# Optimization experiments

Hardware: AMD Instinct MI355X
Metric: run time of the kernel (lower is better)

## Reference

```python
import jax, jax.numpy as jnp
import numpy as np

# Config (matches init_kwargs defaults): V=25 joints, C=16 -> D=400, heads=2,
# ffn=64*25=1600, window L=9, stride=1, postnorm, gelu, dropout ignored (eval).
N, C, T, V = 16, 16, 300, 25
D = C * V          # 400
H = 2              # nhead
FF = 64 * V        # 1600
L = 9              # trans_length
MAX_LEN = 301


def _layernorm(x, g, b, eps=1e-5):
    mu = jnp.mean(x, axis=-1, keepdims=True)
    var = jnp.mean(jnp.square(x - mu), axis=-1, keepdims=True)
    return (x - mu) * jax.lax.rsqrt(var + eps) * g + b


def setup_inputs() -> dict:
    key = jax.random.key(0)
    ks = jax.random.split(key, 12)
    s = 0.02
    return {
        "x": jax.random.normal(ks[0], (N, C, T, V), jnp.float32),
        "pe": jax.random.normal(ks[1], (1, MAX_LEN, D), jnp.float32) * s,
        "w_in": jax.random.normal(ks[2], (3 * D, D), jnp.float32) * s,
        "b_in": jnp.zeros((3 * D,), jnp.float32),
        "w_out": jax.random.normal(ks[3], (D, D), jnp.float32) * s,
        "b_out": jnp.zeros((D,), jnp.float32),
        "w1": jax.random.normal(ks[4], (FF, D), jnp.float32) * s,
        "b1": jnp.zeros((FF,), jnp.float32),
        "w2": jax.random.normal(ks[5], (D, FF), jnp.float32) * s,
        "b2": jnp.zeros((D,), jnp.float32),
        "ln1_g": jnp.ones((D,), jnp.float32),
        "ln1_b": jnp.zeros((D,), jnp.float32),
        "ln2_g": jnp.ones((D,), jnp.float32),
        "ln2_b": jnp.zeros((D,), jnp.float32),
    }


def _encoder_layer(h, w_in, b_in, w_out, b_out, w1, b1, w2, b2,
                   ln1_g, ln1_b, ln2_g, ln2_b):
    # h: [B, L, D]; post-norm TransformerEncoderLayer (torch default)
    B, Lw, Dm = h.shape
    dh = Dm // H
    qkv = h @ w_in.T + b_in                             # [B,L,3D]
    q, k, v = jnp.split(qkv, 3, axis=-1)
    def heads(t):
        return t.reshape(B, Lw, H, dh).transpose(0, 2, 1, 3)  # [B,H,L,dh]
    q, k, v = heads(q), heads(k), heads(v)
    scores = jnp.einsum('bhqd,bhkd->bhqk', q, k) / np.float32(np.sqrt(dh))
    att = jax.nn.softmax(scores, axis=-1)
    o = jnp.einsum('bhqk,bhkd->bhqd', att, v)
    o = o.transpose(0, 2, 1, 3).reshape(B, Lw, Dm) @ w_out.T + b_out
    h = _layernorm(h + o, ln1_g, ln1_b)
    ff = jax.nn.gelu(h @ w1.T + b1, approximate=False) @ w2.T + b2
    return _layernorm(h + ff, ln2_g, ln2_b)


def reference(x, pe, w_in, b_in, w_out, b_out, w1, b1, w2, b2,
              ln1_g, ln1_b, ln2_g, ln2_b):
    n, c, t, v = x.shape
    d = c * v
    # [N,C,T,V] -> [N,T,V,C] -> [N,T,D]  (flatten order is (V,C), as in torch view)
    xs = x.transpose(0, 2, 3, 1).reshape(n, t, d)
    xs = xs + pe[:, :t, :]
    W = t - L                                            # number of windows (stride=1)
    win = jnp.arange(W)
    idx = win[:, None] + jnp.arange(L)[None, :]          # [W,L] gather indices
    xw = xs[:, idx, :].reshape(n * W, L, d)              # batched windows
    out = _encoder_layer(xw, w_in, b_in, w_out, b_out, w1, b1, w2, b2,
                         ln1_g, ln1_b, ln2_g, ln2_b)
    out = out.reshape(n, W * L, d)
    # window i writes into rows i//2 : i//2 + L and results are summed
    pos = ((win // 2)[:, None] + jnp.arange(L)[None, :]).reshape(-1)  # [W*L]
    xt = jnp.zeros((n, t, d), xs.dtype).at[:, pos, :].add(out)
    # [N,T,D] -> [N,T,V,C] -> [N,C,T,V]
    return xt.reshape(n, t, v, c).transpose(0, 3, 1, 2)
```

## Files before the change

### kernel.cpp

```cpp
#include <hip/hip_runtime.h>
#include <cstdint>
#include <cstddef>

#define N_    16
#define C_    16
#define T_    300
#define V_    25
#define D_    400
#define H_    2
#define DH_   200
#define FF_   1600
#define L_    9
#define W_    291
#define NW_   (N_*W_)
#define NT_   (N_*T_)

#define KP_   416
#define SD_   400
#define SQKV_ 1200
#define SFF_  1600

#define WIN_OFF   0u
#define WOUT_OFF  1064960u
#define W1_OFF    1490944u
#define W2_OFF    2981888u
#define XS_OFF    4620288u
#define QKV_OFF   8511488u
#define Z_OFF     20185088u
#define HEAD_END  53708288u

#define WAIT_VM3   0xF73
#define WAIT_VM0   0xF70

using u16 = unsigned short;
using u32 = unsigned int;
using frag  = __attribute__((ext_vector_type(8))) short;
using f32x4 = __attribute__((ext_vector_type(4))) float;

__device__ __forceinline__ float bf2f(u16 u){
  return __uint_as_float(((u32)u) << 16);
}
__device__ __forceinline__ u16 f2bf(float f){
  return (u16)((__float_as_uint(f) + 0x8000u) >> 16);
}
__device__ __forceinline__ u16 f2h(float f){
  _Float16 h = (_Float16)f;
  return *(u16*)&h;
}
__device__ __forceinline__ float h2f(u16 u){
  _Float16 h = *(_Float16*)&u;
  return (float)h;
}
__device__ __forceinline__ float gelu_f(float v){
  float s = __expf(-1.702f * v);
  return v * __builtin_amdgcn_rcpf(1.f + s);
}
__device__ __forceinline__ void unpack8(uint4 v, float* o){
  o[0] = bf2f((u16)(v.x & 0xffffu)); o[1] = bf2f((u16)(v.x >> 16));
  o[2] = bf2f((u16)(v.y & 0xffffu)); o[3] = bf2f((u16)(v.y >> 16));
  o[4] = bf2f((u16)(v.z & 0xffffu)); o[5] = bf2f((u16)(v.z >> 16));
  o[6] = bf2f((u16)(v.w & 0xffffu)); o[7] = bf2f((u16)(v.w >> 16));
}

__device__ __forceinline__ void convw_body(const float* src, u16* dst,
                                           int dN, int dK, int sN, int sK, int idx){
  if (idx >= dN * dK) return;
  int n = idx / dK, k = idx % dK;
  dst[idx] = (n < sN && k < sK) ? f2bf(src[(size_t)n * sK + k]) : (u16)0;
}

#define PREP_GRID 16524
__global__ __launch_bounds__(256) void prep_kernel(const float* __restrict__ x,
                                                   const float* __restrict__ pe,
                                                   const float* __restrict__ w_in,
                                                   const float* __restrict__ w_out,
                                                   const float* __restrict__ w1,
                                                   const float* __restrict__ w2,
                                                   u16* __restrict__ xs,
                                                   u16* __restrict__ w_in_b,
                                                   u16* __restrict__ w_out_b,
                                                   u16* __restrict__ w1_b,
                                                   u16* __restrict__ w2_b){
  int b = blockIdx.x;
  int tid = threadIdx.x;
  if (b < 7500){
    int idx = b * 256 + tid;
    if (idx < NT_ * D_){
      int d  = idx % D_;
      int nt = idx / D_;
      int t  = nt % T_;
      int n  = nt / T_;
      float val = x[(((size_t)(n*C_ + (d & 15)))*T_ + t)*V_ + (d >> 4)] + pe[t*D_ + d];
      xs[idx] = f2bf(val);
    }
  } else if (b < 9580){
    convw_body(w_in,  w_in_b,  1280, KP_, 1200, D_,  (b - 7500) * 256 + tid);
  } else if (b < 10412){
    convw_body(w_out, w_out_b,  512, KP_,  400, D_,  (b - 9580) * 256 + tid);
  } else if (b < 13324){
    convw_body(w1,    w1_b,   1792, KP_, 1600, D_,  (b - 10412) * 256 + tid);
  } else {
    convw_body(w2,    w2_b,    512, SFF_, 400, FF_, (b - 13324) * 256 + tid);
  }
}

template<int ACT>
__global__ __launch_bounds__(512) void gemm_mfma(const u16* __restrict__ A, int lda,
                                                 const u16* __restrict__ B, int ldb,
                                                 const float* __restrict__ bias,
                                                 u16* __restrict__ C, int ldc,
                                                 int Nn, int KPd,
                                                 int gx, int gy){
  __shared__ u16 smem[36864];
  int id = blockIdx.x;
  int c  = id & 7, t = id >> 3;
  int bx = t % gx;
  int by = (t / gx) * 8 + c;
  if (by >= gy) return;
  const int m0 = by * 128, n0 = bx * 256;

  const int tid  = threadIdx.x;
  const int lane = tid & 63;
  const int wv   = tid >> 6;
  const int quad = lane >> 4, l16 = lane & 15;
  const int wm   = wv & 1,   wn  = wv >> 1;

  const int srow = tid >> 2;
  const int sseg = (tid & 3) ^ ((tid >> 3) & 3);
  const u16* Ag = A + (size_t)(m0 + srow) * lda + sseg*8;
  const u16* Bg = B + (size_t)(n0 + srow) * ldb + sseg*8;

  f32x4 acc[4][4] = {};
  const int sa = quad ^ ((l16 >> 1) & 3);

  auto stage = [&](int buf, int kt){
    __builtin_amdgcn_global_load_lds(
        (const __attribute__((address_space(1))) void*)(Ag + kt),
        (__attribute__((address_space(3))) void*)(&smem[buf*4096 + wv*512]), 16, 0, 0);
    __builtin_amdgcn_global_load_lds(
        (const __attribute__((address_space(1))) void*)(Bg + kt),
        (__attribute__((address_space(3))) void*)(&smem[12288 + buf*8192 + wv*512]), 16, 0, 0);
    __builtin_amdgcn_global_load_lds(
        (const __attribute__((address_space(1))) void*)(Bg + kt + (size_t)128*ldb),
        (__attribute__((address_space(3))) void*)(&smem[12288 + buf*8192 + 4096 + wv*512]), 16, 0, 0);
  };

  const int nit = KPd >> 5;
  stage(0, 0);
  stage(1, 32);
  int nb = 2;
  for (int it = 0; it < nit; ++it){
    if (it < nit - 1) __builtin_amdgcn_s_waitcnt(WAIT_VM3);
    else              __builtin_amdgcn_s_waitcnt(WAIT_VM0);
    __builtin_amdgcn_s_barrier();
    if (it + 2 < nit){
      stage(nb, (it + 2) << 5);
      nb = (nb == 2) ? 0 : nb + 1;
    }
    const int buf = it % 3;
    const u16* Ar = &smem[buf*4096];
    const u16* Br = &smem[12288 + buf*8192];
    frag af[4], bfr[4];
    #pragma unroll
    for (int i = 0; i < 4; ++i)
      af[i]  = *(const frag*)(&Ar[(wm*64 + i*16 + l16)*32 + sa*8]);
    #pragma unroll
    for (int j = 0; j < 4; ++j)
      bfr[j] = *(const frag*)(&Br[(wn*64 + j*16 + l16)*32 + sa*8]);
    #pragma unroll
    for (int i = 0; i < 4; ++i)
      #pragma unroll
      for (int j = 0; j < 4; ++j)
        acc[i][j] = __builtin_amdgcn_mfma_f32_16x16x32_bf16(af[i], bfr[j], acc[i][j], 0, 0, 0);
  }

  __builtin_amdgcn_s_barrier();

  u16* ep = &smem[wv * 4608];
  #pragma unroll
  for (int j = 0; j < 4; ++j){
    int n = n0 + wn*64 + j*16 + l16;
    float bj = (n < Nn) ? bias[n] : 0.f;
    #pragma unroll
    for (int i = 0; i < 4; ++i){
      #pragma unroll
      for (int r = 0; r < 4; ++r){
        float v = acc[i][j][r] + bj;
        if (ACT) v = gelu_f(v);
        ep[(i*16 + quad*4 + r)*72 + j*16 + l16] = f2bf(v);
      }
    }
  }
  #pragma unroll
  for (int p = 0; p < 8; ++p){
    int row = p*8 + (lane >> 3);
    int seg = lane & 7;
    int nc  = n0 + wn*64 + seg*8;
    if (nc < Nn){
      uint4 v = *(const uint4*)(&ep[row*72 + seg*8]);
      *(uint4*)(C + (size_t)(m0 + wm*64 + row)*ldc + nc) = v;
    }
  }
}

#define WB_     8
#define ATT_NB  37
#define ATT_GRID (N_ * ATT_NB)
__global__ __launch_bounds__(256) void attn_kernel(const u16* __restrict__ qkv,
                                                   u16* __restrict__ o,
                                                   int g0, int gend){
  __shared__ u16 kv[20480];
  __shared__ float att[WB_ * 2 * 81];
  const int b  = blockIdx.x;
  const int n  = b / ATT_NB;
  const int w0 = (b - n * ATT_NB) * WB_;
  const int gbase = n * W_ + w0;
  if (gbase >= gend || gbase + WB_ <= g0) return;

  const int tid  = threadIdx.x;
  const int lane = tid & 63;
  const int wv   = tid >> 6;

  const char* gsrc = (const char*)(qkv + (size_t)(n * T_ + w0) * SQKV_);
  #pragma unroll
  for (int j = 0; j < 10; ++j){
    __builtin_amdgcn_global_load_lds(
        (const __attribute__((address_space(1))) void*)(gsrc + j*4096 + wv*1024 + lane*16),
        (__attribute__((address_space(3))) void*)((char*)kv + j*4096 + wv*1024),
        16, 0, 0);
  }
  __builtin_amdgcn_s_waitcnt(WAIT_VM0);
  __syncthreads();

  for (int i = tid; i < WB_ * 162; i += 256){
    int w  = i / 162;
    int r  = i - w * 162;
    int h  = r / 81;
    int p  = r - h * 81;
    int qi = p / 9, ki = p - qi * 9;
    const u16* qp = kv + (w + qi) * 1200 + h * DH_;
    const u16* kp = kv + (w + ki) * 1200 + D_ + h * DH_;
    float s = 0.f;
    #pragma unroll 5
    for (int cch = 0; cch < 25; ++cch){
      float qa[8], kb[8];
      unpack8(*(const uint4*)(qp + cch*8), qa);
      unpack8(*(const uint4*)(kp + cch*8), kb);
      #pragma unroll
      for (int e = 0; e < 8; ++e) s += qa[e] * kb[e];
    }
    att[i] = s * 0.07071067811865475f;
  }
  __syncthreads();

  if (tid < WB_ * 18){
    float* row = att + tid * 9;
    float mx = row[0];
    #pragma unroll
    for (int j = 1; j < 9; ++j) mx = fmaxf(mx, row[j]);
    float e[9]; float sum = 0.f;
    #pragma unroll
    for (int j = 0; j < 9; ++j){ e[j] = __expf(row[j] - mx); sum += e[j]; }
    float inv = 1.f / sum;
    #pragma unroll
    for (int j = 0; j < 9; ++j) row[j] = e[j] * inv;
  }
  __syncthreads();

  for (int i = tid; i < WB_ * 900; i += 256){
    int w  = i / 900;
    int r  = i - w * 900;
    int l  = r / 100;
    int c4 = r - l * 100;
    int h  = (c4 >= 50) ? 1 : 0;
    const float* ap = att + (w*2 + h)*81 + l*9;
    float o4[4] = {0.f, 0.f, 0.f, 0.f};
    #pragma unroll
    for (int ki = 0; ki < 9; ++ki){
      float a = ap[ki];
      uint2 vv = *(const uint2*)(kv + (w + ki)*1200 + 2*D_ + c4*4);
      o4[0] += a * bf2f((u16)(vv.x & 0xffffu));
      o4[1] += a * bf2f((u16)(vv.x >> 16));
      o4[2] += a * bf2f((u16)(vv.y & 0xffffu));
      o4[3] += a * bf2f((u16)(vv.y >> 16));
    }
    int g = gbase + w;
    if (w0 + w < W_ && g >= g0 && g < gend){
      u32 lo = (u32)f2bf(o4[0]) | ((u32)f2bf(o4[1]) << 16);
      u32 hi = (u32)f2bf(o4[2]) | ((u32)f2bf(o4[3]) << 16);
      *(uint2*)(o + ((size_t)(g - g0) * L_ + l) * SD_ + c4*4) = make_uint2(lo, hi);
    }
  }
}

__global__ __launch_bounds__(256) void ln1_kernel(const u16* __restrict__ y,
                                                  const float* __restrict__ gam,
                                                  const float* __restrict__ bet,
                                                  u16* __restrict__ out,
                                                  const u16* __restrict__ xs,
                                                  int g0){
  const int wv = threadIdx.x >> 6, lane = threadIdx.x & 63;
  const int r = blockIdx.x * 4 + wv;
  const int g = g0 + r / L_, l = r % L_;
  const int n = g / W_, w = g % W_;
  const u16* arow = xs + ((size_t)(n*T_ + w + l)) * SD_;
  const u16* brow = y + (size_t)r * SD_;

  const bool act = lane < 50;
  float v[8];
  float s = 0.f, s2 = 0.f;
  if (act){
    float a8[8], b8[8];
    unpack8(*(const uint4*)(arow + lane*8), a8);
    unpack8(*(const uint4*)(brow + lane*8), b8);
    #pragma unroll
    for (int i = 0; i < 8; ++i){ v[i] = a8[i] + b8[i]; s += v[i]; s2 += v[i]*v[i]; }
  } else {
    #pragma unroll
    for (int i = 0; i < 8; ++i) v[i] = 0.f;
  }
  #pragma unroll
  for (int off = 32; off; off >>= 1){
    s  += __shfl_xor(s,  off);
    s2 += __shfl_xor(s2, off);
  }
  float mean = s * (1.f / D_);
  float rstd = rsqrtf(s2 * (1.f / D_) - mean*mean + 1e-5f);
  if (act){
    float4 ga = *(const float4*)(gam + lane*8);
    float4 gb = *(const float4*)(gam + lane*8 + 4);
    float4 ba = *(const float4*)(bet + lane*8);
    float4 bb = *(const float4*)(bet + lane*8 + 4);
    float gg[8] = {ga.x,ga.y,ga.z,ga.w, gb.x,gb.y,gb.z,gb.w};
    float bb8[8]= {ba.x,ba.y,ba.z,ba.w, bb.x,bb.y,bb.z,bb.w};
    u32 o4[4];
    #pragma unroll
    for (int i = 0; i < 4; ++i){
      u16 lo = f2bf((v[2*i]   - mean) * rstd * gg[2*i]   + bb8[2*i]);
      u16 hi = f2bf((v[2*i+1] - mean) * rstd * gg[2*i+1] + bb8[2*i+1]);
      o4[i] = (u32)lo | ((u32)hi << 16);
    }
    *(uint4*)(out + (size_t)r * SD_ + lane*8) = make_uint4(o4[0],o4[1],o4[2],o4[3]);
  }
}

__global__ __launch_bounds__(256) void ln2_gather(const u16* __restrict__ h,
                                                  const u16* __restrict__ y,
                                                  const float* __restrict__ gam,
                                                  const float* __restrict__ bet,
                                                  float* __restrict__ dout){
  __shared__ float buf[4][400];
  const int b = blockIdx.x;
  const int t = b % T_;
  const int n = b / T_;
  const int wv = threadIdx.x >> 6, lane = threadIdx.x & 63;
  const bool act = lane < 50;

  float gg[8], bb8[8];
  if (act){
    float4 ga = *(const float4*)(gam + lane*8);
    float4 gb = *(const float4*)(gam + lane*8 + 4);
    float4 ba = *(const float4*)(bet + lane*8);
    float4 bb = *(const float4*)(bet + lane*8 + 4);
    gg[0]=ga.x; gg[1]=ga.y; gg[2]=ga.z; gg[3]=ga.w;
    gg[4]=gb.x; gg[5]=gb.y; gg[6]=gb.z; gg[7]=gb.w;
    bb8[0]=ba.x; bb8[1]=ba.y; bb8[2]=ba.z; bb8[3]=ba.w;
    bb8[4]=bb.x; bb8[5]=bb.y; bb8[6]=bb.z; bb8[7]=bb.w;
  }
  float racc[8] = {0.f,0.f,0.f,0.f,0.f,0.f,0.f,0.f};

  for (int idx = wv; idx < 18; idx += 4){
    int l  = idx >> 1;
    int dt = t - l;
    if (dt < 0 || dt > 145) continue;
    int w = dt * 2 + (idx & 1);
    if (w >= W_) continue;
    size_t r = ((size_t)(n * W_ + w)) * L_ + l;
    const u16* arow = h + r * SD_;
    const u16* brow = y + r * SD_;
    float v[8];
    float s = 0.f, s2 = 0.f;
    if (act){
      float a8[8], b8[8];
      unpack8(*(const uint4*)(arow + lane*8), a8);
      unpack8(*(const uint4*)(brow + lane*8), b8);
      #pragma unroll
      for (int i = 0; i < 8; ++i){ v[i] = a8[i] + b8[i]; s += v[i]; s2 += v[i]*v[i]; }
    } else {
      #pragma unroll
      for (int i = 0; i < 8; ++i) v[i] = 0.f;
    }
    #pragma unroll
    for (int off = 32; off; off >>= 1){
      s  += __shfl_xor(s,  off);
      s2 += __shfl_xor(s2, off);
    }
    float mean = s * (1.f / D_);
    float rstd = rsqrtf(s2 * (1.f / D_) - mean*mean + 1e-5f);
    if (act){
      #pragma unroll
      for (int i = 0; i < 8; ++i)
        racc[i] += (v[i] - mean) * rstd * gg[i] + bb8[i];
    }
  }
  if (act){
    #pragma unroll
    for (int i = 0; i < 8; ++i) buf[wv][lane*8 + i] = racc[i];
  }
  __syncthreads();
  for (int d = threadIdx.x; d < D_; d += 256){
    float s = buf[0][d] + buf[1][d] + buf[2][d] + buf[3][d];
    dout[(((size_t)(n*C_ + (d & 15)))*T_ + t)*V_ + (d >> 4)] = s;
  }
}

__global__ __launch_bounds__(256) void ln2z_kernel(const u16* __restrict__ h,
                                                   const u16* __restrict__ y,
                                                   const float* __restrict__ gam,
                                                   const float* __restrict__ bet,
                                                   u16* __restrict__ z,
                                                   int g0){
  const int wv = threadIdx.x >> 6, lane = threadIdx.x & 63;
  const int r = blockIdx.x * 4 + wv;
  const u16* arow = h + (size_t)r * SD_;
  const u16* brow = y + (size_t)r * SD_;

  const bool act = lane < 50;
  float v[8];
  float s = 0.f, s2 = 0.f;
  if (act){
    float a8[8], b8[8];
    unpack8(*(const uint4*)(arow + lane*8), a8);
    unpack8(*(const uint4*)(brow + lane*8), b8);
    #pragma unroll
    for (int i = 0; i < 8; ++i){ v[i] = a8[i] + b8[i]; s += v[i]; s2 += v[i]*v[i]; }
  } else {
    #pragma unroll
    for (int i = 0; i < 8; ++i) v[i] = 0.f;
  }
  #pragma unroll
  for (int off = 32; off; off >>= 1){
    s  += __shfl_xor(s,  off);
    s2 += __shfl_xor(s2, off);
  }
  float mean = s * (1.f / D_);
  float rstd = rsqrtf(s2 * (1.f / D_) - mean*mean + 1e-5f);
  if (act){
    float4 ga = *(const float4*)(gam + lane*8);
    float4 gb = *(const float4*)(gam + lane*8 + 4);
    float4 ba = *(const float4*)(bet + lane*8);
    float4 bb = *(const float4*)(bet + lane*8 + 4);
    float gg[8] = {ga.x,ga.y,ga.z,ga.w, gb.x,gb.y,gb.z,gb.w};
    float bb8[8]= {ba.x,ba.y,ba.z,ba.w, bb.x,bb.y,bb.z,bb.w};
    u32 o4[4];
    #pragma unroll
    for (int i = 0; i < 4; ++i){
      u16 lo = f2h((v[2*i]   - mean) * rstd * gg[2*i]   + bb8[2*i]);
      u16 hi = f2h((v[2*i+1] - mean) * rstd * gg[2*i+1] + bb8[2*i+1]);
      o4[i] = (u32)lo | ((u32)hi << 16);
    }
    *(uint4*)(z + ((size_t)(g0 * L_) + r) * SD_ + lane*8) = make_uint4(o4[0],o4[1],o4[2],o4[3]);
  }
}

__global__ __launch_bounds__(256) void gather_final(const u16* __restrict__ z,
                                                    float* __restrict__ dout){
  int idx = blockIdx.x * 256 + threadIdx.x;
  if (idx >= NT_ * D_) return;
  int d  = idx % D_;
  int nt = idx / D_;
  int t  = nt % T_;
  int n  = nt / T_;
  float s = 0.f;
  #pragma unroll
  for (int l = 0; l < L_; ++l){
    int dt = t - l;
    if (dt >= 0 && dt <= 145){
      int w = dt * 2;
      const u16* zp = z + ((size_t)((n*W_ + w)*L_ + l)) * SD_ + d;
      s += h2f(zp[0]);
      if (w + 1 < W_) s += h2f(zp[(size_t)L_ * SD_]);
    }
  }
  dout[(((size_t)(n*C_ + (d & 15)))*T_ + t)*V_ + (d >> 4)] = s;
}

extern "C" void kernel_launch(void* const* d_in, const int* in_sizes, int n_in,
                              void* d_out, int out_size, void* d_ws, size_t ws_size,
                              hipStream_t stream){
  (void)in_sizes; (void)n_in; (void)out_size;
  const float* x     = (const float*)d_in[0];
  const float* pe    = (const float*)d_in[1];
  const float* w_in  = (const float*)d_in[2];
  const float* b_in  = (const float*)d_in[3];
  const float* w_out = (const float*)d_in[4];
  const float* b_out = (const float*)d_in[5];
  const float* w1    = (const float*)d_in[6];
  const float* b1    = (const float*)d_in[7];
  const float* w2    = (const float*)d_in[8];
  const float* b2    = (const float*)d_in[9];
  const float* ln1g  = (const float*)d_in[10];
  const float* ln1b  = (const float*)d_in[11];
  const float* ln2g  = (const float*)d_in[12];
  const float* ln2b  = (const float*)d_in[13];

  int nch = 3;
  {
    size_t need1 = (size_t)HEAD_END + (size_t)41984 * 4800;
    size_t need2 = (size_t)HEAD_END + (size_t)20992 * 4800;
    if (ws_size >= need1 + (1u<<20)) nch = 1;
    else if (ws_size >= need2 + (1u<<20)) nch = 2;
  }
  const int CW  = NW_ / nch;
  const int RC  = CW * L_;
  const int RCP = ((RC + 127) / 128) * 128;

  char* ws = (char*)d_ws;
  u16*   w_in_b  = (u16*)(ws + WIN_OFF);
  u16*   w_out_b = (u16*)(ws + WOUT_OFF);
  u16*   w1_b    = (u16*)(ws + W1_OFF);
  u16*   w2_b    = (u16*)(ws + W2_OFF);
  u16*   xs      = (u16*)(ws + XS_OFF);
  u16*   qkv     = (u16*)(ws + QKV_OFF);
  u16*   z       = (u16*)(ws + Z_OFF);
  u16*   y_c     = (u16*)(ws + HEAD_END);
  u16*   h_c     = y_c + (size_t)RCP * SD_;
  u16*   ffc     = h_c + (size_t)RCP * SD_;
  u16*   o_c     = ffc;

  prep_kernel<<<PREP_GRID, 256, 0, stream>>>(x, pe, w_in, w_out, w1, w2,
                                             xs, w_in_b, w_out_b, w1_b, w2_b);

  {
    int gx = 5, gy = (NT_ + 127)/128, gy8 = (gy + 7) & ~7;
    gemm_mfma<0><<<gx*gy8, 512, 0, stream>>>(
        xs, SD_, w_in_b, KP_, b_in, qkv, SQKV_, 1200, KP_, gx, gy);
  }

  const int gyc = RCP/128, gyc8 = (gyc + 7) & ~7;

  for (int g0 = 0; g0 < NW_; g0 += CW){
    attn_kernel<<<ATT_GRID, 256, 0, stream>>>(qkv, o_c, g0, g0 + CW);

    gemm_mfma<0><<<2*gyc8, 512, 0, stream>>>(
        o_c, SD_, w_out_b, KP_, b_out, y_c, SD_, D_, KP_, 2, gyc);

    ln1_kernel<<<RC/4, 256, 0, stream>>>(y_c, ln1g, ln1b, h_c, xs, g0);

    gemm_mfma<1><<<7*gyc8, 512, 0, stream>>>(
        h_c, SD_, w1_b, KP_, b1, ffc, SFF_, FF_, KP_, 7, gyc);

    gemm_mfma<0><<<2*gyc8, 512, 0, stream>>>(
        ffc, SFF_, w2_b, SFF_, b2, y_c, SD_, D_, SFF_, 2, gyc);

    if (nch > 1)
      ln2z_kernel<<<RC/4, 256, 0, stream>>>(h_c, y_c, ln2g, ln2b, z, g0);
  }

  if (nch == 1)
    ln2_gather<<<NT_, 256, 0, stream>>>(h_c, y_c, ln2g, ln2b, (float*)d_out);
  else
    gather_final<<<(NT_*D_ + 255)/256, 256, 0, stream>>>(z, (float*)d_out);
}
```

Baseline: 356.9 us.

## Split FF2 GEMM along K into two halves and coalesce prep transpose via LDS

The second FFN GEMM (K=1600) is split into two K-halves run as separate blocks, which doubles the block count. Each half writes its own bf16 partial output, and ln2_gather sums the two partials along with the residual. The split targets low occupancy, since the 2-column-tile GEMM launches few blocks for a large K. Separately, the input transpose in prep_kernel now reads one (n,t) slice into shared memory before writing xs, so the scattered global reads become staged ones. The cost is extra partial-sum traffic and an extra bf16 rounding of each partial, and the partial buffer y2 reuses the z region.

```diff
diff --git a/kernel.cpp b/kernel.cpp
--- a/kernel.cpp
+++ b/kernel.cpp
@@ -69,7 +69,7 @@
   dst[idx] = (n < sN && k < sK) ? f2bf(src[(size_t)n * sK + k]) : (u16)0;
 }
 
-#define PREP_GRID 16524
+#define PREP_GRID 13824
 __global__ __launch_bounds__(256) void prep_kernel(const float* __restrict__ x,
                                                    const float* __restrict__ pe,
                                                    const float* __restrict__ w_in,
@@ -81,26 +81,28 @@
                                                    u16* __restrict__ w_out_b,
                                                    u16* __restrict__ w1_b,
                                                    u16* __restrict__ w2_b){
+  __shared__ float xv[400];
   int b = blockIdx.x;
   int tid = threadIdx.x;
-  if (b < 7500){
-    int idx = b * 256 + tid;
-    if (idx < NT_ * D_){
-      int d  = idx % D_;
-      int nt = idx / D_;
-      int t  = nt % T_;
-      int n  = nt / T_;
-      float val = x[(((size_t)(n*C_ + (d & 15)))*T_ + t)*V_ + (d >> 4)] + pe[t*D_ + d];
-      xs[idx] = f2bf(val);
-    }
-  } else if (b < 9580){
-    convw_body(w_in,  w_in_b,  1280, KP_, 1200, D_,  (b - 7500) * 256 + tid);
-  } else if (b < 10412){
-    convw_body(w_out, w_out_b,  512, KP_,  400, D_,  (b - 9580) * 256 + tid);
-  } else if (b < 13324){
-    convw_body(w1,    w1_b,   1792, KP_, 1600, D_,  (b - 10412) * 256 + tid);
+  if (b < 4800){
+    int t = b % T_, n = b / T_;
+    for (int i = tid; i < 400; i += 256){
+      int c = i / 25, v = i - c*25;
+      xv[i] = x[(((size_t)(n*C_ + c))*T_ + t)*V_ + v];
+    }
+    __syncthreads();
+    for (int d = tid; d < 400; d += 256){
+      float val = xv[(d & 15)*25 + (d >> 4)] + pe[t*D_ + d];
+      xs[(size_t)b * D_ + d] = f2bf(val);
+    }
+  } else if (b < 6880){
+    convw_body(w_in,  w_in_b,  1280, KP_, 1200, D_,  (b - 4800) * 256 + tid);
+  } else if (b < 7712){
+    convw_body(w_out, w_out_b,  512, KP_,  400, D_,  (b - 6880) * 256 + tid);
+  } else if (b < 10624){
+    convw_body(w1,    w1_b,   1792, KP_, 1600, D_,  (b - 7712) * 256 + tid);
   } else {
-    convw_body(w2,    w2_b,    512, SFF_, 400, FF_, (b - 13324) * 256 + tid);
+    convw_body(w2,    w2_b,    512, SFF_, 400, FF_, (b - 10624) * 256 + tid);
   }
 }
 
@@ -203,6 +205,108 @@
   }
 }
 
+__global__ __launch_bounds__(512) void gemm_ff2(const u16* __restrict__ A, int lda,
+                                                const u16* __restrict__ B, int ldb,
+                                                const float* __restrict__ bias,
+                                                u16* __restrict__ C0, u16* __restrict__ C1,
+                                                int ldc, int Nn, int KH,
+                                                int gx, int gy, int Mr){
+  __shared__ u16 smem[36864];
+  int id = blockIdx.x;
+  int c  = id & 7, t = id >> 3;
+  int bxp = t % (2*gx);
+  int by  = (t / (2*gx)) * 8 + c;
+  if (by >= gy) return;
+  const int half = (bxp >= gx) ? 1 : 0;
+  const int bx   = bxp - half*gx;
+  const int m0 = by * 128, n0 = bx * 256;
+  const int koff = half * KH;
+  u16* C = half ? C1 : C0;
+
+  const int tid  = threadIdx.x;
+  const int lane = tid & 63;
+  const int wv   = tid >> 6;
+  const int quad = lane >> 4, l16 = lane & 15;
+  const int wm   = wv & 1,   wn  = wv >> 1;
+
+  const int srow = tid >> 2;
+  const int sseg = (tid & 3) ^ ((tid >> 3) & 3);
+  const u16* Ag = A + (size_t)(m0 + srow) * lda + koff + sseg*8;
+  const u16* Bg = B + (size_t)(n0 + srow) * ldb + koff + sseg*8;
+
+  f32x4 acc[4][4] = {};
+  const int sa = quad ^ ((l16 >> 1) & 3);
+
+  auto stage = [&](int buf, int kt){
+    __builtin_amdgcn_global_load_lds(
+        (const __attribute__((address_space(1))) void*)(Ag + kt),
+        (__attribute__((address_space(3))) void*)(&smem[buf*4096 + wv*512]), 16, 0, 0);
+    __builtin_amdgcn_global_load_lds(
+        (const __attribute__((address_space(1))) void*)(Bg + kt),
+        (__attribute__((address_space(3))) void*)(&smem[12288 + buf*8192 + wv*512]), 16, 0, 0);
+    __builtin_amdgcn_global_load_lds(
+        (const __attribute__((address_space(1))) void*)(Bg + kt + (size_t)128*ldb),
+        (__attribute__((address_space(3))) void*)(&smem[12288 + buf*8192 + 4096 + wv*512]), 16, 0, 0);
+  };
+
+  const int nit = KH >> 5;
+  stage(0, 0);
+  stage(1, 32);
+  int nb = 2;
+  for (int it = 0; it < nit; ++it){
+    if (it < nit - 1) __builtin_amdgcn_s_waitcnt(WAIT_VM3);
+    else              __builtin_amdgcn_s_waitcnt(WAIT_VM0);
+    __builtin_amdgcn_s_barrier();
+    if (it + 2 < nit){
+      stage(nb, (it + 2) << 5);
+      nb = (nb == 2) ? 0 : nb + 1;
+    }
+    const int buf = it % 3;
+    const u16* Ar = &smem[buf*4096];
+    const u16* Br = &smem[12288 + buf*8192];
+    frag af[4], bfr[4];
+    #pragma unroll
+    for (int i = 0; i < 4; ++i)
+      af[i]  = *(const frag*)(&Ar[(wm*64 + i*16 + l16)*32 + sa*8]);
+    #pragma unroll
+    for (int j = 0; j < 4; ++j)
+      bfr[j] = *(const frag*)(&Br[(wn*64 + j*16 + l16)*32 + sa*8]);
+    #pragma unroll
+    for (int i = 0; i < 4; ++i)
+      #pragma unroll
+      for (int j = 0; j < 4; ++j)
+        acc[i][j] = __builtin_amdgcn_mfma_f32_16x16x32_bf16(af[i], bfr[j], acc[i][j], 0, 0, 0);
+  }
+
+  __builtin_amdgcn_s_barrier();
+
+  u16* ep = &smem[wv * 4608];
+  #pragma unroll
+  for (int j = 0; j < 4; ++j){
+    int n = n0 + wn*64 + j*16 + l16;
+    float bj = (!half && n < Nn) ? bias[n] : 0.f;
+    #pragma unroll
+    for (int i = 0; i < 4; ++i){
+      #pragma unroll
+      for (int r = 0; r < 4; ++r){
+        float v = acc[i][j][r] + bj;
+        ep[(i*16 + quad*4 + r)*72 + j*16 + l16] = f2bf(v);
+      }
+    }
+  }
+  #pragma unroll
+  for (int p = 0; p < 8; ++p){
+    int row = p*8 + (lane >> 3);
+    int seg = lane & 7;
+    int nc  = n0 + wn*64 + seg*8;
+    int mr  = m0 + wm*64 + row;
+    if (nc < Nn && mr < Mr){
+      uint4 v = *(const uint4*)(&ep[row*72 + seg*8]);
+      *(uint4*)(C + (size_t)mr*ldc + nc) = v;
+    }
+  }
+}
+
 #define WB_     8
 #define ATT_NB  37
 #define ATT_GRID (N_ * ATT_NB)
@@ -346,6 +450,7 @@
 
 __global__ __launch_bounds__(256) void ln2_gather(const u16* __restrict__ h,
                                                   const u16* __restrict__ y,
+                                                  const u16* __restrict__ y2,
                                                   const float* __restrict__ gam,
                                                   const float* __restrict__ bet,
                                                   float* __restrict__ dout){
@@ -378,14 +483,16 @@
     size_t r = ((size_t)(n * W_ + w)) * L_ + l;
     const u16* arow = h + r * SD_;
     const u16* brow = y + r * SD_;
+    const u16* crow = y2 + r * SD_;
     float v[8];
     float s = 0.f, s2 = 0.f;
     if (act){
-      float a8[8], b8[8];
+      float a8[8], b8[8], c8[8];
       unpack8(*(const uint4*)(arow + lane*8), a8);
       unpack8(*(const uint4*)(brow + lane*8), b8);
-      #pragma unroll
-      for (int i = 0; i < 8; ++i){ v[i] = a8[i] + b8[i]; s += v[i]; s2 += v[i]*v[i]; }
+      unpack8(*(const uint4*)(crow + lane*8), c8);
+      #pragma unroll
+      for (int i = 0; i < 8; ++i){ v[i] = a8[i] + b8[i] + c8[i]; s += v[i]; s2 += v[i]*v[i]; }
     } else {
       #pragma unroll
       for (int i = 0; i < 8; ++i) v[i] = 0.f;
@@ -523,6 +630,7 @@
   u16*   xs      = (u16*)(ws + XS_OFF);
   u16*   qkv     = (u16*)(ws + QKV_OFF);
   u16*   z       = (u16*)(ws + Z_OFF);
+  u16*   y2      = (u16*)(ws + Z_OFF);
   u16*   y_c     = (u16*)(ws + HEAD_END);
   u16*   h_c     = y_c + (size_t)RCP * SD_;
   u16*   ffc     = h_c + (size_t)RCP * SD_;
@@ -550,15 +658,18 @@
     gemm_mfma<1><<<7*gyc8, 512, 0, stream>>>(
         h_c, SD_, w1_b, KP_, b1, ffc, SFF_, FF_, KP_, 7, gyc);
 
-    gemm_mfma<0><<<2*gyc8, 512, 0, stream>>>(
-        ffc, SFF_, w2_b, SFF_, b2, y_c, SD_, D_, SFF_, 2, gyc);
-
-    if (nch > 1)
+    if (nch == 1){
+      gemm_ff2<<<4*gyc8, 512, 0, stream>>>(
+          ffc, SFF_, w2_b, SFF_, b2, y_c, y2, SD_, D_, 800, 2, gyc, RC);
+    } else {
+      gemm_mfma<0><<<2*gyc8, 512, 0, stream>>>(
+          ffc, SFF_, w2_b, SFF_, b2, y_c, SD_, D_, SFF_, 2, gyc);
       ln2z_kernel<<<RC/4, 256, 0, stream>>>(h_c, y_c, ln2g, ln2b, z, g0);
+    }
   }
 
   if (nch == 1)
-    ln2_gather<<<NT_, 256, 0, stream>>>(h_c, y_c, ln2g, ln2b, (float*)d_out);
+    ln2_gather<<<NT_, 256, 0, stream>>>(h_c, y_c, y2, ln2g, ln2b, (float*)d_out);
   else
     gather_final<<<(NT_*D_ + 255)/256, 256, 0, stream>>>(z, (float*)d_out);
 }
```

Result: slower. 364.5 us (+2.1%).
